# Optimization experiments

Measured on AMD Instinct MI355X. Metric: run time of the kernel, lower is better.

The kernel has to match this reference:

```python
import jax, jax.numpy as jnp
import numpy as np

H = 8  # number of heads


def setup_inputs() -> dict:
    key = jax.random.key(0)
    ks = jax.random.split(key, 5)
    B, L, D = 4, 2048, 512
    scale = 1.0 / np.sqrt(D)
    return {
        "query": jax.random.normal(ks[0], (B, L, D), dtype=jnp.float32),
        "keys": jax.random.normal(ks[1], (B, L, D), dtype=jnp.float32),
        "Wq": jax.random.normal(ks[2], (D, D), dtype=jnp.float32) * scale,
        "Wk": jax.random.normal(ks[3], (D, D), dtype=jnp.float32) * scale,
        "Wv": jax.random.normal(ks[4], (D, D), dtype=jnp.float32) * scale,
    }


def reference(query, keys, Wq, Wk, Wv):
    B, Lq, D = query.shape
    Lk = keys.shape[1]
    dh = D // H
    # Linear layers (torch nn.Linear: y = x @ W.T), then split heads.
    Q = (query @ Wq.T).reshape(B, Lq, H, dh)
    K = (keys @ Wk.T).reshape(B, Lk, H, dh)
    V = (keys @ Wv.T).reshape(B, Lk, H, dh)
    # NOTE: original scales by sqrt(key_dim) == sqrt(D), not sqrt(head_dim).
    inv_scale = 1.0 / jnp.sqrt(jnp.float32(D))
    scores = jnp.einsum("bqhd,bkhd->bhqk", Q, K) * inv_scale  # [B,H,Lq,Lk]
    attn = jax.nn.softmax(scores, axis=-1)
    # dropout_p = 0 (eval); no dropout applied.
    out = jnp.einsum("bhqk,bkhd->bqhd", attn, V).reshape(B, Lq, D)
    return out + query  # residual
```

## Files before the change

kernel.cpp:

```cpp
#include <hip/hip_runtime.h>

typedef unsigned short u16;
typedef unsigned int   u32;
typedef short  s16x4  __attribute__((ext_vector_type(4)));
typedef short  s16x8  __attribute__((ext_vector_type(8)));
typedef float  f32x16 __attribute__((ext_vector_type(16)));

__device__ __forceinline__ u16 f2bf(float f) {
    union { u32 i; float f; } x; x.f = f;
    return (u16)((x.i + 0x8000u) >> 16);
}
__device__ __forceinline__ u32 pk_hi16(float a, float b) {
    union { float f; u32 u; } ua, ub; ua.f = a; ub.f = b;
    return __builtin_amdgcn_perm(ub.u + 0x8000u, ua.u + 0x8000u, 0x07060302u);
}

#if __has_builtin(__builtin_amdgcn_mfma_f32_32x32x8bf16_1k)
#define HAVE_X8 1
#define MFMA8(a, b, c) __builtin_amdgcn_mfma_f32_32x32x8bf16_1k((a), (b), (c), 0, 0, 0)
#elif __has_builtin(__builtin_amdgcn_mfma_f32_32x32x8_bf16)
#define HAVE_X8 1
#define MFMA8(a, b, c) __builtin_amdgcn_mfma_f32_32x32x8_bf16((a), (b), (c), 0, 0, 0)
#else
#define HAVE_X8 0
#endif

#define PD 512

__global__ __launch_bounds__(256) void proj_mfma(
    const float* __restrict__ query, const float* __restrict__ keys,
    const float* __restrict__ Wq, const float* __restrict__ Wk, const float* __restrict__ Wv,
    u16* __restrict__ Qo, u16* __restrict__ Ko, u16* __restrict__ Vt)
{
    const int z = blockIdx.z;
    const float* __restrict__ X = (z == 0) ? query : keys;
    const float* __restrict__ W = (z == 0) ? Wq : ((z == 1) ? Wk : Wv);
    const int bx = blockIdx.x;
    const int by = blockIdx.y;

    const float* __restrict__ Amat = (z < 2) ? X : W;
    const float* __restrict__ Bmat = (z < 2) ? W : X;
    const int a0 = ((z < 2) ? bx : by) * 128;
    const int b0 = ((z < 2) ? by : bx) * 128;

    __shared__ u16 As[128][40];
    __shared__ u16 Bs[128][40];

    const int tid  = threadIdx.x;
    const int wave = tid >> 6, lane = tid & 63;
    const int wm = wave >> 1, wn = wave & 1;
    const int l31 = lane & 31, lh = lane >> 5;

    const int srow = tid >> 1;
    const int sk   = (tid & 1) * 16;

    f32x16 acc[2][2];
    #pragma unroll
    for (int i = 0; i < 2; ++i)
        #pragma unroll
        for (int j = 0; j < 2; ++j)
            #pragma unroll
            for (int r = 0; r < 16; ++r) acc[i][j][r] = 0.f;

    float4 ra[4], rb[4];
    {
        const float* ap = Amat + (size_t)(a0 + srow) * PD + sk;
        const float* bp = Bmat + (size_t)(b0 + srow) * PD + sk;
        #pragma unroll
        for (int i = 0; i < 4; ++i) {
            ra[i] = *(const float4*)(ap + 4*i);
            rb[i] = *(const float4*)(bp + 4*i);
        }
    }

    for (int k0 = 0; k0 < PD; k0 += 32) {
        __syncthreads();
        {
            u32 aw[8], bw[8];
            #pragma unroll
            for (int i = 0; i < 4; ++i) {
                aw[2*i]   = pk_hi16(ra[i].x, ra[i].y);
                aw[2*i+1] = pk_hi16(ra[i].z, ra[i].w);
                bw[2*i]   = pk_hi16(rb[i].x, rb[i].y);
                bw[2*i+1] = pk_hi16(rb[i].z, rb[i].w);
            }
            *(uint4*)&As[srow][sk]     = *(uint4*)&aw[0];
            *(uint4*)&As[srow][sk + 8] = *(uint4*)&aw[4];
            *(uint4*)&Bs[srow][sk]     = *(uint4*)&bw[0];
            *(uint4*)&Bs[srow][sk + 8] = *(uint4*)&bw[4];
        }
        if (k0 + 32 < PD) {
            const float* ap = Amat + (size_t)(a0 + srow) * PD + (k0 + 32) + sk;
            const float* bp = Bmat + (size_t)(b0 + srow) * PD + (k0 + 32) + sk;
            #pragma unroll
            for (int i = 0; i < 4; ++i) {
                ra[i] = *(const float4*)(ap + 4*i);
                rb[i] = *(const float4*)(bp + 4*i);
            }
        }
        __syncthreads();

        #pragma unroll
        for (int ks = 0; ks < 2; ++ks) {
            s16x8 af[2], bfr[2];
            #pragma unroll
            for (int mf = 0; mf < 2; ++mf) {
                uint4 v = *(uint4*)&As[wm*64 + mf*32 + l31][ks*16 + lh*8];
                af[mf] = *(s16x8*)&v;
            }
            #pragma unroll
            for (int nf = 0; nf < 2; ++nf) {
                uint4 v = *(uint4*)&Bs[wn*64 + nf*32 + l31][ks*16 + lh*8];
                bfr[nf] = *(s16x8*)&v;
            }
            #pragma unroll
            for (int mf = 0; mf < 2; ++mf)
                #pragma unroll
                for (int nf = 0; nf < 2; ++nf)
                    acc[mf][nf] = __builtin_amdgcn_mfma_f32_32x32x16_bf16(
                        af[mf], bfr[nf], acc[mf][nf], 0, 0, 0);
        }
    }

    const float osc = (z == 0) ? (0.044194173824159216f * 1.4426950408889634f) : 1.0f;
    u16* __restrict__ O = (z == 0) ? Qo : Ko;
    #pragma unroll
    for (int mf = 0; mf < 2; ++mf)
        #pragma unroll
        for (int nf = 0; nf < 2; ++nf)
            #pragma unroll
            for (int r = 0; r < 16; ++r) {
                const int mi = a0 + wm*64 + mf*32 + (r & 3) + 8*(r >> 2) + 4*lh;
                const int ni = b0 + wn*64 + nf*32 + l31;
                const u16 v = f2bf(acc[mf][nf][r] * osc);
                if (z < 2) {
                    O[(size_t)mi * PD + ni] = v;
                } else {
                    const int bb_ = ni >> 11, ll = ni & 2047;
                    Vt[((size_t)(bb_ * 512 + mi)) * 2048 + ll] = v;
                }
            }
}

__global__ __launch_bounds__(256) void attn_mfma(
    const u16* __restrict__ Qp, const u16* __restrict__ Kp, const u16* __restrict__ Vt,
    const float* __restrict__ query, float* __restrict__ out)
{
    const int qt = blockIdx.x;
    const int h  = blockIdx.y;
    const int b  = blockIdx.z;
    const int q0 = qt * 128;
    const int L = 2048;

    __shared__ uint4 lds_u4[36864 / 16];
    u16* Ks   = (u16*)lds_u4;
    u16* Vts  = Ks + 64 * 72;
#if !HAVE_X8
    u16* P2a  = Vts + 64 * 72;
#endif
    float* Oe = (float*)lds_u4;

    const int tid  = threadIdx.x;
    const int wave = tid >> 6, lane = tid & 63;
    const int l31 = lane & 31, lh = lane >> 5;
#if !HAVE_X8
    u16* P2 = P2a + wave * 32 * 72;
#endif

    const int qrow = b * L + q0 + wave * 32 + l31;
    s16x8 qf[4];
    #pragma unroll
    for (int ds = 0; ds < 4; ++ds) {
        uint4 v = *(const uint4*)(Qp + (size_t)qrow * PD + h*64 + ds*16 + lh*8);
        qf[ds] = *(s16x8*)&v;
    }

    f32x16 ot[2];
    #pragma unroll
    for (int mf = 0; mf < 2; ++mf)
        #pragma unroll
        for (int r = 0; r < 16; ++r) ot[mf][r] = 0.f;
    float l_i = 0.f;

    const int srow = tid >> 2;
    const int sc   = (tid & 3) * 16;

    uint4 rk0, rk1, rv0, rv1;
    {
        const u16* kp = Kp + (size_t)(b*L + srow) * PD + h*64 + sc;
        const u16* vp = Vt + ((size_t)((b*8 + h)*64 + srow)) * 2048 + sc;
        rk0 = *(const uint4*)kp;      rk1 = *(const uint4*)(kp + 8);
        rv0 = *(const uint4*)vp;      rv1 = *(const uint4*)(vp + 8);
    }

    for (int k0 = 0; k0 < L; k0 += 64) {
        __syncthreads();
        *(uint4*)&Ks [srow*72 + sc]     = rk0;
        *(uint4*)&Ks [srow*72 + sc + 8] = rk1;
        *(uint4*)&Vts[srow*72 + sc]     = rv0;
        *(uint4*)&Vts[srow*72 + sc + 8] = rv1;
        if (k0 + 64 < L) {
            const u16* kp = Kp + (size_t)(b*L + (k0+64) + srow) * PD + h*64 + sc;
            const u16* vp = Vt + ((size_t)((b*8 + h)*64 + srow)) * 2048 + (k0+64) + sc;
            rk0 = *(const uint4*)kp;  rk1 = *(const uint4*)(kp + 8);
            rv0 = *(const uint4*)vp;  rv1 = *(const uint4*)(vp + 8);
        }
        __syncthreads();

        f32x16 s[2];
        #pragma unroll
        for (int kf = 0; kf < 2; ++kf) {
            #pragma unroll
            for (int r = 0; r < 16; ++r) s[kf][r] = 0.f;
            #pragma unroll
            for (int ds = 0; ds < 4; ++ds) {
                uint4 av = *(uint4*)&Ks[(kf*32 + l31)*72 + ds*16 + lh*8];
                s[kf] = __builtin_amdgcn_mfma_f32_32x32x16_bf16(
                    *(s16x8*)&av, qf[ds], s[kf], 0, 0, 0);
            }
        }

        float rs = 0.f;
        u32 pq[2][4][2];
        #pragma unroll
        for (int kf = 0; kf < 2; ++kf)
            #pragma unroll
            for (int g = 0; g < 4; ++g) {
                float p0 = __builtin_amdgcn_exp2f(s[kf][4*g+0]);
                float p1 = __builtin_amdgcn_exp2f(s[kf][4*g+1]);
                float p2 = __builtin_amdgcn_exp2f(s[kf][4*g+2]);
                float p3 = __builtin_amdgcn_exp2f(s[kf][4*g+3]);
                rs += (p0 + p1) + (p2 + p3);
                pq[kf][g][0] = pk_hi16(p0, p1);
                pq[kf][g][1] = pk_hi16(p2, p3);
#if !HAVE_X8
                uint2 w2; w2.x = pq[kf][g][0]; w2.y = pq[kf][g][1];
                *(uint2*)&P2[l31*72 + kf*32 + g*8 + lh*4] = w2;
#endif
            }
        rs += __shfl_xor(rs, 32);
        l_i += rs;

#if HAVE_X8
        #pragma unroll
        for (int kf = 0; kf < 2; ++kf)
            #pragma unroll
            for (int g = 0; g < 4; ++g) {
                union { u32 w[2]; s16x4 v; } bu;
                bu.w[0] = pq[kf][g][0];
                bu.w[1] = pq[kf][g][1];
                #pragma unroll
                for (int mf = 0; mf < 2; ++mf) {
                    union { uint2 u; s16x4 v; } au;
                    au.u = *(uint2*)&Vts[(mf*32 + l31)*72 + kf*32 + g*8 + lh*4];
                    ot[mf] = MFMA8(au.v, bu.v, ot[mf]);
                }
            }
#else
        #pragma unroll
        for (int ks = 0; ks < 4; ++ks) {
            uint4 bv = *(uint4*)&P2[l31*72 + ks*16 + lh*8];
            s16x8 bfr = *(s16x8*)&bv;
            #pragma unroll
            for (int mf = 0; mf < 2; ++mf) {
                uint4 av = *(uint4*)&Vts[(mf*32 + l31)*72 + ks*16 + lh*8];
                ot[mf] = __builtin_amdgcn_mfma_f32_32x32x16_bf16(
                    *(s16x8*)&av, bfr, ot[mf], 0, 0, 0);
            }
        }
#endif
    }

    __syncthreads();
    const float inv_l = 1.0f / l_i;
    #pragma unroll
    for (int mf = 0; mf < 2; ++mf)
        #pragma unroll
        for (int g = 0; g < 4; ++g) {
            float4 v;
            v.x = ot[mf][g*4+0] * inv_l;
            v.y = ot[mf][g*4+1] * inv_l;
            v.z = ot[mf][g*4+2] * inv_l;
            v.w = ot[mf][g*4+3] * inv_l;
            const int dh0 = mf*32 + 8*g + 4*lh;
            *(float4*)&Oe[(wave*32 + l31)*68 + dh0] = v;
        }
    __syncthreads();
    {
        const int r  = tid >> 1;
        const int c0 = (tid & 1) * 32;
        const size_t gb = ((size_t)(b*L + q0 + r)) * PD + h*64 + c0;
        #pragma unroll
        for (int i = 0; i < 8; ++i) {
            float4 ov = *(float4*)&Oe[r*68 + c0 + 4*i];
            float4 qv = *(const float4*)(query + gb + 4*i);
            ov.x += qv.x; ov.y += qv.y; ov.z += qv.z; ov.w += qv.w;
            *(float4*)(out + gb + 4*i) = ov;
        }
    }
}

extern "C" void kernel_launch(void* const* d_in, const int* in_sizes, int n_in,
                              void* d_out, int out_size, void* d_ws, size_t ws_size,
                              hipStream_t stream) {
    const float* query = (const float*)d_in[0];
    const float* keys  = (const float*)d_in[1];
    const float* Wq    = (const float*)d_in[2];
    const float* Wk    = (const float*)d_in[3];
    const float* Wv    = (const float*)d_in[4];
    float* out = (float*)d_out;

    u16* Qp = (u16*)d_ws;
    u16* Kp = Qp + (size_t)8192 * 512;
    u16* Vt = Kp + (size_t)8192 * 512;

    proj_mfma<<<dim3(64, 4, 3), 256, 0, stream>>>(query, keys, Wq, Wk, Wv, Qp, Kp, Vt);
    attn_mfma<<<dim3(16, 8, 4), 256, 0, stream>>>(Qp, Kp, Vt, query, out);
}
```

Baseline: 171.9 us.

## Halve attention block to two waves and swizzle LDS K/V tiles

Result: slower. 271.5 us (+58.0%).

```diff
diff --git a/kernel.cpp b/kernel.cpp
--- a/kernel.cpp
+++ b/kernel.cpp
@@ -142,30 +142,24 @@
             }
 }
 
-__global__ __launch_bounds__(256) void attn_mfma(
+__global__ __launch_bounds__(128) void attn_mfma(
     const u16* __restrict__ Qp, const u16* __restrict__ Kp, const u16* __restrict__ Vt,
     const float* __restrict__ query, float* __restrict__ out)
 {
     const int qt = blockIdx.x;
     const int h  = blockIdx.y;
     const int b  = blockIdx.z;
-    const int q0 = qt * 128;
+    const int q0 = qt * 64;
     const int L = 2048;
 
-    __shared__ uint4 lds_u4[36864 / 16];
-    u16* Ks   = (u16*)lds_u4;
-    u16* Vts  = Ks + 64 * 72;
-#if !HAVE_X8
-    u16* P2a  = Vts + 64 * 72;
-#endif
-    float* Oe = (float*)lds_u4;
+    __shared__ u32 lds_raw[17408 / 4];
+    u16* Ks   = (u16*)lds_raw;
+    u16* Vts  = Ks + 64 * 64;
+    float* Oe = (float*)lds_raw;
 
     const int tid  = threadIdx.x;
     const int wave = tid >> 6, lane = tid & 63;
     const int l31 = lane & 31, lh = lane >> 5;
-#if !HAVE_X8
-    u16* P2 = P2a + wave * 32 * 72;
-#endif
 
     const int qrow = b * L + q0 + wave * 32 + l31;
     s16x8 qf[4];
@@ -182,28 +176,38 @@
         for (int r = 0; r < 16; ++r) ot[mf][r] = 0.f;
     float l_i = 0.f;
 
-    const int srow = tid >> 2;
-    const int sc   = (tid & 3) * 16;
-
-    uint4 rk0, rk1, rv0, rv1;
+    const int srow = tid >> 1;
+    const int shalf = tid & 1;
+    const int sxor = (srow & 7) << 3;
+
+    uint4 rk[4], rv[4];
     {
-        const u16* kp = Kp + (size_t)(b*L + srow) * PD + h*64 + sc;
-        const u16* vp = Vt + ((size_t)((b*8 + h)*64 + srow)) * 2048 + sc;
-        rk0 = *(const uint4*)kp;      rk1 = *(const uint4*)(kp + 8);
-        rv0 = *(const uint4*)vp;      rv1 = *(const uint4*)(vp + 8);
+        const u16* kp = Kp + (size_t)(b*L + srow) * PD + h*64 + shalf*32;
+        const u16* vp = Vt + ((size_t)((b*8 + h)*64 + srow)) * 2048 + shalf*32;
+        #pragma unroll
+        for (int i = 0; i < 4; ++i) {
+            rk[i] = *(const uint4*)(kp + 8*i);
+            rv[i] = *(const uint4*)(vp + 8*i);
+        }
     }
 
     for (int k0 = 0; k0 < L; k0 += 64) {
         __syncthreads();
-        *(uint4*)&Ks [srow*72 + sc]     = rk0;
-        *(uint4*)&Ks [srow*72 + sc + 8] = rk1;
-        *(uint4*)&Vts[srow*72 + sc]     = rv0;
-        *(uint4*)&Vts[srow*72 + sc + 8] = rv1;
+        #pragma unroll
+        for (int i = 0; i < 4; ++i) {
+            const int c = shalf*4 + i;
+            const int po = srow*64 + (((c << 3) ) ^ sxor);
+            *(uint4*)&Ks [po] = rk[i];
+            *(uint4*)&Vts[po] = rv[i];
+        }
         if (k0 + 64 < L) {
-            const u16* kp = Kp + (size_t)(b*L + (k0+64) + srow) * PD + h*64 + sc;
-            const u16* vp = Vt + ((size_t)((b*8 + h)*64 + srow)) * 2048 + (k0+64) + sc;
-            rk0 = *(const uint4*)kp;  rk1 = *(const uint4*)(kp + 8);
-            rv0 = *(const uint4*)vp;  rv1 = *(const uint4*)(vp + 8);
+            const u16* kp = Kp + (size_t)(b*L + (k0+64) + srow) * PD + h*64 + shalf*32;
+            const u16* vp = Vt + ((size_t)((b*8 + h)*64 + srow)) * 2048 + (k0+64) + shalf*32;
+            #pragma unroll
+            for (int i = 0; i < 4; ++i) {
+                rk[i] = *(const uint4*)(kp + 8*i);
+                rv[i] = *(const uint4*)(vp + 8*i);
+            }
         }
         __syncthreads();
 
@@ -214,7 +218,8 @@
             for (int r = 0; r < 16; ++r) s[kf][r] = 0.f;
             #pragma unroll
             for (int ds = 0; ds < 4; ++ds) {
-                uint4 av = *(uint4*)&Ks[(kf*32 + l31)*72 + ds*16 + lh*8];
+                const int row = kf*32 + l31;
+                uint4 av = *(uint4*)&Ks[row*64 + ((((ds*2 + lh) << 3)) ^ ((row & 7) << 3))];
                 s[kf] = __builtin_amdgcn_mfma_f32_32x32x16_bf16(
                     *(s16x8*)&av, qf[ds], s[kf], 0, 0, 0);
             }
@@ -233,10 +238,6 @@
                 rs += (p0 + p1) + (p2 + p3);
                 pq[kf][g][0] = pk_hi16(p0, p1);
                 pq[kf][g][1] = pk_hi16(p2, p3);
-#if !HAVE_X8
-                uint2 w2; w2.x = pq[kf][g][0]; w2.y = pq[kf][g][1];
-                *(uint2*)&P2[l31*72 + kf*32 + g*8 + lh*4] = w2;
-#endif
             }
         rs += __shfl_xor(rs, 32);
         l_i += rs;
@@ -251,23 +252,38 @@
                 bu.w[1] = pq[kf][g][1];
                 #pragma unroll
                 for (int mf = 0; mf < 2; ++mf) {
+                    const int row = mf*32 + l31;
                     union { uint2 u; s16x4 v; } au;
-                    au.u = *(uint2*)&Vts[(mf*32 + l31)*72 + kf*32 + g*8 + lh*4];
+                    au.u = *(uint2*)&Vts[row*64 + ((((kf*4 + g) << 3)) ^ ((row & 7) << 3)) + lh*4];
                     ot[mf] = MFMA8(au.v, bu.v, ot[mf]);
                 }
             }
 #else
         #pragma unroll
-        for (int ks = 0; ks < 4; ++ks) {
-            uint4 bv = *(uint4*)&P2[l31*72 + ks*16 + lh*8];
-            s16x8 bfr = *(s16x8*)&bv;
-            #pragma unroll
-            for (int mf = 0; mf < 2; ++mf) {
-                uint4 av = *(uint4*)&Vts[(mf*32 + l31)*72 + ks*16 + lh*8];
-                ot[mf] = __builtin_amdgcn_mfma_f32_32x32x16_bf16(
-                    *(s16x8*)&av, bfr, ot[mf], 0, 0, 0);
-            }
-        }
+        for (int kf = 0; kf < 2; ++kf)
+            #pragma unroll
+            for (int t = 0; t < 2; ++t) {
+                const int g_own  = 2*t + lh;
+                const int g_send = 2*t + (lh ^ 1);
+                const u32 sx = __shfl_xor((int)pq[kf][g_send][0], 32);
+                const u32 sy = __shfl_xor((int)pq[kf][g_send][1], 32);
+                const u32 ox = pq[kf][g_own][0], oy = pq[kf][g_own][1];
+                union { u32 w[4]; s16x8 v; } bu;
+                bu.w[0] = lh ? sx : ox;
+                bu.w[1] = lh ? sy : oy;
+                bu.w[2] = lh ? ox : sx;
+                bu.w[3] = lh ? oy : sy;
+                #pragma unroll
+                for (int mf = 0; mf < 2; ++mf) {
+                    const int row = mf*32 + l31;
+                    const int c0 = kf*4 + t*2;
+                    union { uint2 u[2]; s16x8 v; } au;
+                    au.u[0] = *(uint2*)&Vts[row*64 + (((c0 + 0) << 3) ^ ((row & 7) << 3)) + lh*4];
+                    au.u[1] = *(uint2*)&Vts[row*64 + (((c0 + 1) << 3) ^ ((row & 7) << 3)) + lh*4];
+                    ot[mf] = __builtin_amdgcn_mfma_f32_32x32x16_bf16(
+                        au.v, bu.v, ot[mf], 0, 0, 0);
+                }
+            }
 #endif
     }
 
@@ -315,5 +331,5 @@
     u16* Vt = Kp + (size_t)8192 * 512;
 
     proj_mfma<<<dim3(64, 4, 3), 256, 0, stream>>>(query, keys, Wq, Wk, Wv, Qp, Kp, Vt);
-    attn_mfma<<<dim3(16, 8, 4), 256, 0, stream>>>(Qp, Kp, Vt, query, out);
-}
+    attn_mfma<<<dim3(32, 8, 4), 128, 0, stream>>>(Qp, Kp, Vt, query, out);
+}
```
